# Kernel optimization log

Measured on AMD Instinct MI355X. Metric: run time of the kernel, lower is better.

Reference implementation:

```python
import jax, jax.numpy as jnp
import numpy as np

B, T, C = 2, 2048, 2048
H, HKV = 32, 8
D = C // H            # head_dim = 64
G = H // HKV          # groups = 4
ROPE_BASE = 10000.0


def _rotate_half(x):
    x1, x2 = jnp.split(x, 2, axis=-1)
    return jnp.concatenate((-x2, x1), axis=-1)


def _rope_tables(seq_len, dim):
    inv_freq = 1.0 / (ROPE_BASE ** (jnp.arange(0, dim, 2, dtype=jnp.float32) / dim))
    t = jnp.arange(seq_len, dtype=jnp.float32)
    freqs = jnp.outer(t, inv_freq)          # [T, D/2]
    emb = jnp.concatenate((freqs, freqs), axis=-1)  # [T, D]
    return jnp.cos(emb), jnp.sin(emb)


def setup_inputs() -> dict:
    key = jax.random.key(0)
    ks = jax.random.split(key, 5)
    s = 0.02
    return {
        "x": jax.random.normal(ks[0], (B, T, C), jnp.float32),
        "Wq": jax.random.normal(ks[1], (C, C), jnp.float32) * s,
        "Wk": jax.random.normal(ks[2], (HKV * D, C), jnp.float32) * s,
        "Wv": jax.random.normal(ks[3], (HKV * D, C), jnp.float32) * s,
        "Wo": jax.random.normal(ks[4], (C, C), jnp.float32) * s,
    }


def reference(x, Wq, Wk, Wv, Wo):
    b, t, c = x.shape
    # fused QKV projections (nn.Linear: y = x @ W.T)
    q = (x @ Wq.T).reshape(b, t, H, D).transpose(0, 2, 1, 3)      # [B,H,T,D]
    k = (x @ Wk.T).reshape(b, t, HKV, D).transpose(0, 2, 1, 3)    # [B,HKV,T,D]
    v = (x @ Wv.T).reshape(b, t, HKV, D).transpose(0, 2, 1, 3)

    # RoPE (start_pos = 0)
    cos, sin = _rope_tables(t, D)           # [T, D] each
    cos = cos[None, None]                   # [1,1,T,D]
    sin = sin[None, None]
    q = q * cos + _rotate_half(q) * sin
    k = k * cos + _rotate_half(k) * sin

    # GQA head expansion (repeat_interleave on head dim)
    k = jnp.repeat(k, G, axis=1)            # [B,H,T,D]
    v = jnp.repeat(v, G, axis=1)

    # causal attention
    scale = 1.0 / jnp.sqrt(jnp.asarray(D, jnp.float32))
    scores = jnp.einsum('bhqd,bhkd->bhqk', q, k) * scale          # [B,H,T,T]
    causal = jnp.tril(jnp.ones((t, t), dtype=bool))
    scores = jnp.where(causal[None, None], scores, -jnp.inf)
    attn = jax.nn.softmax(scores.astype(jnp.float32), axis=-1).astype(q.dtype)
    out = jnp.einsum('bhqk,bhkd->bhqd', attn, v)                  # [B,H,T,D]
    out = out.transpose(0, 2, 1, 3).reshape(b, t, c)
    return out @ Wo.T
```

## Files before the change

kernel.cpp:

```cpp
#include <hip/hip_runtime.h>
#include <hip/hip_bf16.h>
#include <math.h>

typedef short short8 __attribute__((ext_vector_type(8)));
typedef float floatx4 __attribute__((ext_vector_type(4)));

typedef __attribute__((address_space(1))) unsigned int as1_u32;
typedef __attribute__((address_space(3))) unsigned int as3_u32;

__device__ __forceinline__ void load_lds16(const void* g, void* l) {
  __builtin_amdgcn_global_load_lds((const as1_u32*)g, (as3_u32*)l, 16, 0, 0);
}

__device__ __forceinline__ unsigned short f2bf(float f) {
  __bf16 h = (__bf16)f;
  return __builtin_bit_cast(unsigned short, h);
}

#define TB 2
#define TT 2048
#define TC 2048
#define QKN 2560
#define KOFF 2048
#define SCALE_Q 0.18033688f

__global__ __launch_bounds__(256) void cast_all(
    const float* __restrict__ x, const float* __restrict__ wq,
    const float* __restrict__ wk, const float* __restrict__ wv,
    const float* __restrict__ wo,
    unsigned short* __restrict__ xb, unsigned short* __restrict__ wqkv,
    unsigned short* __restrict__ wob) {
  long i4 = (long)blockIdx.x * 256 + threadIdx.x;
  const float* src;
  unsigned short* dst;
  if (i4 < 2097152)      { src = x;  dst = xb; }
  else if (i4 < 3145728) { src = wq; dst = wqkv;           i4 -= 2097152; }
  else if (i4 < 3407872) { src = wk; dst = wqkv + 4194304; i4 -= 3145728; }
  else if (i4 < 3670016) { src = wv; dst = wqkv + 5242880; i4 -= 3407872; }
  else                   { src = wo; dst = wob;            i4 -= 3670016; }
  float4 v = ((const float4*)src)[i4];
  ushort4 o;
  o.x = f2bf(v.x); o.y = f2bf(v.y); o.z = f2bf(v.z); o.w = f2bf(v.w);
  ((ushort4*)dst)[i4] = o;
}

__global__ __launch_bounds__(256) void gemm_qkv(const unsigned short* __restrict__ A,
                                                const unsigned short* __restrict__ Bw,
                                                unsigned short* __restrict__ qk,
                                                unsigned short* __restrict__ vT) {
  __shared__ unsigned short As[128 * 64];
  __shared__ unsigned short Bs[128 * 64];
  const int K = 2048;
  const int tid = threadIdx.x;
  const int lane = tid & 63, w = tid >> 6;
  const int quad = lane >> 4, l15 = lane & 15;
  const int wm = w >> 1, wn = w & 1;
  const int m0 = blockIdx.y * 128, n0 = blockIdx.x * 128;

  floatx4 acc[4][4];
#pragma unroll
  for (int i = 0; i < 4; ++i)
#pragma unroll
    for (int j = 0; j < 4; ++j) acc[i][j] = (floatx4){0.f, 0.f, 0.f, 0.f};

  const int ar = tid >> 3;
  const int ac = (((tid & 7) ^ (ar & 7)) * 8);
  const unsigned short* Abase = A + (size_t)(m0 + ar) * K + ac;
  const unsigned short* Bbase = Bw + (size_t)(n0 + ar) * K + ac;

  for (int k0 = 0; k0 < K; k0 += 64) {
    __syncthreads();
#pragma unroll
    for (int p = 0; p < 4; ++p) {
      load_lds16(Abase + (size_t)(p * 32) * K + k0, (char*)As + p * 4096 + tid * 16);
      load_lds16(Bbase + (size_t)(p * 32) * K + k0, (char*)Bs + p * 4096 + tid * 16);
    }
    __syncthreads();
#pragma unroll
    for (int ks = 0; ks < 2; ++ks) {
      short8 af[4], bfr[4];
      const int key = (((ks << 2) + quad) ^ (l15 & 7)) << 4;
#pragma unroll
      for (int i = 0; i < 4; ++i)
        af[i] = *(const short8*)((const char*)As + (wm * 64 + i * 16 + l15) * 128 + key);
#pragma unroll
      for (int j = 0; j < 4; ++j)
        bfr[j] = *(const short8*)((const char*)Bs + (wn * 64 + j * 16 + l15) * 128 + key);
#pragma unroll
      for (int i = 0; i < 4; ++i)
#pragma unroll
        for (int j = 0; j < 4; ++j)
          acc[i][j] = __builtin_amdgcn_mfma_f32_16x16x32_bf16(af[i], bfr[j], acc[i][j], 0, 0, 0);
    }
  }

  const int colb = n0 + wn * 64;
  if (colb < QKN) {
    const float qscale = (colb < KOFF) ? SCALE_Q : 1.0f;
#pragma unroll
    for (int i = 0; i < 4; ++i) {
      const int rowb = m0 + wm * 64 + i * 16 + quad * 4;
      const int tb = rowb & (TT - 1);
#pragma unroll
      for (int j = 0; j < 2; ++j) {
        const int col = colb + j * 16 + l15;
        const int d = j * 16 + l15;
        const float inv = exp2f((float)d * -0.4152410119f);
#pragma unroll
        for (int r = 0; r < 4; ++r) {
          float sn, cs;
          sincosf((float)(tb + r) * inv, &sn, &cs);
          const float a = acc[i][j][r], b2 = acc[i][j + 2][r];
          const float qa = (a * cs - b2 * sn) * qscale;
          const float qb = (b2 * cs + a * sn) * qscale;
          unsigned short* p = qk + (size_t)(rowb + r) * QKN + col;
          p[0] = f2bf(qa);
          p[32] = f2bf(qb);
        }
      }
    }
  } else {
#pragma unroll
    for (int i = 0; i < 4; ++i) {
      const int rowb = m0 + wm * 64 + i * 16 + quad * 4;
#pragma unroll
      for (int j = 0; j < 4; ++j) {
        const int col = colb + j * 16 + l15;
        ushort4 pk;
        pk.x = f2bf(acc[i][j][0]); pk.y = f2bf(acc[i][j][1]);
        pk.z = f2bf(acc[i][j][2]); pk.w = f2bf(acc[i][j][3]);
        *(ushort4*)(vT + (size_t)(col - 2560) * 4096 + rowb) = pk;
      }
    }
  }
}

__global__ __launch_bounds__(256) void gemm_nt_f32(const unsigned short* __restrict__ A,
                                                   const unsigned short* __restrict__ Bw,
                                                   float* __restrict__ C,
                                                   int M, int N, int K) {
  __shared__ unsigned short As[128 * 64];
  __shared__ unsigned short Bs[128 * 64];
  const int tid = threadIdx.x;
  const int lane = tid & 63, w = tid >> 6;
  const int quad = lane >> 4, l15 = lane & 15;
  const int wm = w >> 1, wn = w & 1;
  const int m0 = blockIdx.y * 128, n0 = blockIdx.x * 128;

  floatx4 acc[4][4];
#pragma unroll
  for (int i = 0; i < 4; ++i)
#pragma unroll
    for (int j = 0; j < 4; ++j) acc[i][j] = (floatx4){0.f, 0.f, 0.f, 0.f};

  const int ar = tid >> 3;
  const int ac = (((tid & 7) ^ (ar & 7)) * 8);
  const unsigned short* Abase = A + (size_t)(m0 + ar) * K + ac;
  const unsigned short* Bbase = Bw + (size_t)(n0 + ar) * K + ac;

  for (int k0 = 0; k0 < K; k0 += 64) {
    __syncthreads();
#pragma unroll
    for (int p = 0; p < 4; ++p) {
      load_lds16(Abase + (size_t)(p * 32) * K + k0, (char*)As + p * 4096 + tid * 16);
      load_lds16(Bbase + (size_t)(p * 32) * K + k0, (char*)Bs + p * 4096 + tid * 16);
    }
    __syncthreads();
#pragma unroll
    for (int ks = 0; ks < 2; ++ks) {
      short8 af[4], bfr[4];
      const int key = (((ks << 2) + quad) ^ (l15 & 7)) << 4;
#pragma unroll
      for (int i = 0; i < 4; ++i)
        af[i] = *(const short8*)((const char*)As + (wm * 64 + i * 16 + l15) * 128 + key);
#pragma unroll
      for (int j = 0; j < 4; ++j)
        bfr[j] = *(const short8*)((const char*)Bs + (wn * 64 + j * 16 + l15) * 128 + key);
#pragma unroll
      for (int i = 0; i < 4; ++i)
#pragma unroll
        for (int j = 0; j < 4; ++j)
          acc[i][j] = __builtin_amdgcn_mfma_f32_16x16x32_bf16(af[i], bfr[j], acc[i][j], 0, 0, 0);
    }
  }
#pragma unroll
  for (int i = 0; i < 4; ++i) {
    const int row = m0 + wm * 64 + i * 16 + quad * 4;
#pragma unroll
    for (int j = 0; j < 4; ++j) {
      const int col = n0 + wn * 64 + j * 16 + l15;
#pragma unroll
      for (int r = 0; r < 4; ++r)
        C[(size_t)(row + r) * N + col] = acc[i][j][r];
    }
  }
}

#define LDSA_K(buf) (lds + (buf) * 8192)
#define LDSA_V(buf) (lds + 16384 + (buf) * 8192)
#define LDSA_P      (lds + 32768)

__global__ __launch_bounds__(256) void attn_kernel(const unsigned short* __restrict__ qk,
                                                   const unsigned short* __restrict__ vT,
                                                   unsigned short* __restrict__ attn) {
  const int bx = blockIdx.x;
  const int h = blockIdx.y, b = blockIdx.z;
  const int hk = h >> 2;
  const int tid = threadIdx.x;
  const int w = tid >> 6, lane = tid & 63, quad = lane >> 4, l15 = lane & 15;

  __shared__ char lds[51200];
  unsigned short* Pq = (unsigned short*)(LDSA_P + w * 4608);

  const int srow = tid >> 3;
  const int sgrp = ((tid & 7) ^ (srow & 7));

  const short8 ones = {16256, 16256, 16256, 16256, 16256, 16256, 16256, 16256};

  for (int pass = 0; pass < 2; ++pass) {
    const int qt = pass ? (15 - bx) : bx;
    const size_t rowQ = (size_t)(b * TT + qt * 128);

    {
      const unsigned short* qsrc = qk + (rowQ + srow) * QKN + h * 64 + sgrp * 8;
#pragma unroll
      for (int p = 0; p < 4; ++p)
        load_lds16(qsrc + (size_t)p * 32 * QKN, lds + p * 4096 + tid * 16);
    }
    __syncthreads();
    short8 qf[2][2];
#pragma unroll
    for (int i = 0; i < 2; ++i)
#pragma unroll
      for (int ks = 0; ks < 2; ++ks)
        qf[i][ks] = *(const short8*)(lds + (w * 32 + i * 16 + l15) * 128 +
                                     ((((ks << 2) + quad) ^ (l15 & 7)) << 4));
    __syncthreads();

    floatx4 accO[2][4], accL[2];
#pragma unroll
    for (int i = 0; i < 2; ++i) {
      accL[i] = (floatx4){0.f, 0.f, 0.f, 0.f};
#pragma unroll
      for (int j = 0; j < 4; ++j) accO[i][j] = (floatx4){0.f, 0.f, 0.f, 0.f};
    }

    {
      const unsigned short* ksrc =
          qk + (size_t)(b * TT + srow) * QKN + KOFF + hk * 64 + sgrp * 8;
      load_lds16(ksrc, LDSA_K(0) + tid * 16);
      load_lds16(ksrc + (size_t)32 * QKN, LDSA_K(0) + 4096 + tid * 16);
      const unsigned short* vsrc =
          vT + (size_t)(hk * 64 + srow) * 4096 + b * TT + sgrp * 8;
      load_lds16(vsrc, LDSA_V(0) + tid * 16);
      load_lds16(vsrc + (size_t)32 * 4096, LDSA_V(0) + 4096 + tid * 16);
    }
    __syncthreads();

    const int ktmax = 2 * qt + 1;
    for (int kt = 0; kt <= ktmax; ++kt) {
      const int cur = kt & 1, nxt = cur ^ 1;
      if (kt < ktmax) {
        const unsigned short* ksrc =
            qk + (size_t)(b * TT + (kt + 1) * 64 + srow) * QKN + KOFF + hk * 64 + sgrp * 8;
        load_lds16(ksrc, LDSA_K(nxt) + tid * 16);
        load_lds16(ksrc + (size_t)32 * QKN, LDSA_K(nxt) + 4096 + tid * 16);
        const unsigned short* vsrc =
            vT + (size_t)(hk * 64 + srow) * 4096 + b * TT + (kt + 1) * 64 + sgrp * 8;
        load_lds16(vsrc, LDSA_V(nxt) + tid * 16);
        load_lds16(vsrc + (size_t)32 * 4096, LDSA_V(nxt) + 4096 + tid * 16);
      }

      const char* Ks = LDSA_K(cur);
      floatx4 st[2][4];
#pragma unroll
      for (int jm = 0; jm < 4; ++jm) {
        const int krow = jm * 16 + l15;
        const short8 kf0 = *(const short8*)(Ks + krow * 128 + ((quad ^ (l15 & 7)) << 4));
        const short8 kf1 = *(const short8*)(Ks + krow * 128 + (((4 + quad) ^ (l15 & 7)) << 4));
#pragma unroll
        for (int i = 0; i < 2; ++i) {
          floatx4 z = (floatx4){0.f, 0.f, 0.f, 0.f};
          z = __builtin_amdgcn_mfma_f32_16x16x32_bf16(kf0, qf[i][0], z, 0, 0, 0);
          st[i][jm] = __builtin_amdgcn_mfma_f32_16x16x32_bf16(kf1, qf[i][1], z, 0, 0, 0);
        }
      }

      const bool domask = (kt >= 2 * qt);
#pragma unroll
      for (int i = 0; i < 2; ++i) {
        const int qg = qt * 128 + w * 32 + i * 16 + l15;
#pragma unroll
        for (int jm = 0; jm < 4; ++jm) {
          float e0 = exp2f(st[i][jm][0]);
          float e1 = exp2f(st[i][jm][1]);
          float e2 = exp2f(st[i][jm][2]);
          float e3 = exp2f(st[i][jm][3]);
          if (domask) {
            const int kg = kt * 64 + jm * 16 + quad * 4;
            if (kg > qg) e0 = 0.f;
            if (kg + 1 > qg) e1 = 0.f;
            if (kg + 2 > qg) e2 = 0.f;
            if (kg + 3 > qg) e3 = 0.f;
          }
          ushort4 pk;
          pk.x = f2bf(e0); pk.y = f2bf(e1); pk.z = f2bf(e2); pk.w = f2bf(e3);
          *(ushort4*)(Pq + (i * 16 + l15) * 72 + jm * 16 + quad * 4) = pk;
        }
      }
      asm volatile("s_waitcnt lgkmcnt(0)" ::: "memory");

      const char* Vt = LDSA_V(cur);
#pragma unroll
      for (int ks = 0; ks < 2; ++ks) {
        short8 pf[2];
#pragma unroll
        for (int i2 = 0; i2 < 2; ++i2)
          pf[i2] = *(const short8*)(Pq + (i2 * 16 + l15) * 72 + ks * 32 + quad * 8);
        accL[0] = __builtin_amdgcn_mfma_f32_16x16x32_bf16(pf[0], ones, accL[0], 0, 0, 0);
        accL[1] = __builtin_amdgcn_mfma_f32_16x16x32_bf16(pf[1], ones, accL[1], 0, 0, 0);
#pragma unroll
        for (int jd = 0; jd < 4; ++jd) {
          const int d = jd * 16 + l15;
          const short8 vf = *(const short8*)(Vt + d * 128 +
                                             ((((ks << 2) + quad) ^ (l15 & 7)) << 4));
          accO[0][jd] = __builtin_amdgcn_mfma_f32_16x16x32_bf16(pf[0], vf, accO[0][jd], 0, 0, 0);
          accO[1][jd] = __builtin_amdgcn_mfma_f32_16x16x32_bf16(pf[1], vf, accO[1][jd], 0, 0, 0);
        }
      }
      __syncthreads();
    }

#pragma unroll
    for (int i2 = 0; i2 < 2; ++i2) {
#pragma unroll
      for (int jd = 0; jd < 4; ++jd) {
        const int col = h * 64 + jd * 16 + l15;
#pragma unroll
        for (int r = 0; r < 4; ++r) {
          const size_t row = rowQ + w * 32 + i2 * 16 + quad * 4 + r;
          attn[row * TC + col] = f2bf(accO[i2][jd][r] / accL[i2][r]);
        }
      }
    }
  }
}

extern "C" void kernel_launch(void* const* d_in, const int* in_sizes, int n_in,
                              void* d_out, int out_size, void* d_ws, size_t ws_size,
                              hipStream_t stream) {
  const float* x = (const float*)d_in[0];
  const float* Wq = (const float*)d_in[1];
  const float* Wk = (const float*)d_in[2];
  const float* Wv = (const float*)d_in[3];
  const float* Wo = (const float*)d_in[4];
  float* out = (float*)d_out;

  char* ws = (char*)d_ws;
  unsigned short* xb   = (unsigned short*)(ws);
  unsigned short* wqkv = (unsigned short*)(ws + 16777216);
  unsigned short* wob  = (unsigned short*)(ws + 29360128);
  unsigned short* qk   = (unsigned short*)(ws + 37748736);
  unsigned short* vT   = (unsigned short*)(ws + 58720256);
  unsigned short* attn = (unsigned short*)(ws + 62914560);

  cast_all<<<18432, 256, 0, stream>>>(x, Wq, Wk, Wv, Wo, xb, wqkv, wob);
  gemm_qkv<<<dim3(24, 32), 256, 0, stream>>>(xb, wqkv, qk, vT);
  attn_kernel<<<dim3(8, 32, 2), 256, 0, stream>>>(qk, vT, attn);
  gemm_nt_f32<<<dim3(16, 32), 256, 0, stream>>>(attn, wob, out, 4096, TC, 2048);
}
```

Before: 300.8 us.

## Precompute RoPE table and remap block indices for cache-friendly XCD scheduling

Computes a cos/sin RoPE table once inside the cast kernel and has the QKV GEMM epilogue read it instead of calling sincosf per element. It also remaps the linear block IDs in both GEMMs and the attention kernel. Blocks that share the same A rows or the same KV head then land on the same XCD (assuming round-robin dispatch across 8 XCDs), which improves L2 reuse. The table reuses the attention-output workspace region, which is safe only because attention writes there after the GEMM has consumed the table.

Result: no change. 297.9 us (-1.0%).

```diff
diff --git a/kernel.cpp b/kernel.cpp
--- a/kernel.cpp
+++ b/kernel.cpp
@@ -29,7 +29,15 @@
     const float* __restrict__ wk, const float* __restrict__ wv,
     const float* __restrict__ wo,
     unsigned short* __restrict__ xb, unsigned short* __restrict__ wqkv,
-    unsigned short* __restrict__ wob) {
+    unsigned short* __restrict__ wob, float2* __restrict__ ropeTab) {
+  if (blockIdx.x < 256) {
+    const int idx = blockIdx.x * 256 + threadIdx.x;
+    const int t = idx >> 5, d = idx & 31;
+    const float inv = exp2f((float)d * -0.4152410119f);
+    float sn, cs;
+    sincosf((float)t * inv, &sn, &cs);
+    ropeTab[idx] = make_float2(cs, sn);
+  }
   long i4 = (long)blockIdx.x * 256 + threadIdx.x;
   const float* src;
   unsigned short* dst;
@@ -47,7 +55,8 @@
 __global__ __launch_bounds__(256) void gemm_qkv(const unsigned short* __restrict__ A,
                                                 const unsigned short* __restrict__ Bw,
                                                 unsigned short* __restrict__ qk,
-                                                unsigned short* __restrict__ vT) {
+                                                unsigned short* __restrict__ vT,
+                                                const float2* __restrict__ ropeTab) {
   __shared__ unsigned short As[128 * 64];
   __shared__ unsigned short Bs[128 * 64];
   const int K = 2048;
@@ -55,7 +64,10 @@
   const int lane = tid & 63, w = tid >> 6;
   const int quad = lane >> 4, l15 = lane & 15;
   const int wm = w >> 1, wn = w & 1;
-  const int m0 = blockIdx.y * 128, n0 = blockIdx.x * 128;
+  const int lin = blockIdx.y * 24 + blockIdx.x;
+  const int sub = lin >> 3;
+  const int m0 = (sub / 3) * 128;
+  const int n0 = ((lin & 7) * 3 + sub % 3) * 128;
 
   floatx4 acc[4][4];
 #pragma unroll
@@ -105,14 +117,12 @@
       for (int j = 0; j < 2; ++j) {
         const int col = colb + j * 16 + l15;
         const int d = j * 16 + l15;
-        const float inv = exp2f((float)d * -0.4152410119f);
 #pragma unroll
         for (int r = 0; r < 4; ++r) {
-          float sn, cs;
-          sincosf((float)(tb + r) * inv, &sn, &cs);
+          const float2 cssn = ropeTab[(tb + r) * 32 + d];
           const float a = acc[i][j][r], b2 = acc[i][j + 2][r];
-          const float qa = (a * cs - b2 * sn) * qscale;
-          const float qb = (b2 * cs + a * sn) * qscale;
+          const float qa = (a * cssn.x - b2 * cssn.y) * qscale;
+          const float qb = (b2 * cssn.x + a * cssn.y) * qscale;
           unsigned short* p = qk + (size_t)(rowb + r) * QKN + col;
           p[0] = f2bf(qa);
           p[32] = f2bf(qb);
@@ -145,7 +155,10 @@
   const int lane = tid & 63, w = tid >> 6;
   const int quad = lane >> 4, l15 = lane & 15;
   const int wm = w >> 1, wn = w & 1;
-  const int m0 = blockIdx.y * 128, n0 = blockIdx.x * 128;
+  const int lin = blockIdx.y * 16 + blockIdx.x;
+  const int sub = lin >> 3;
+  const int m0 = (sub >> 1) * 128;
+  const int n0 = ((lin & 7) * 2 + (sub & 1)) * 128;
 
   floatx4 acc[4][4];
 #pragma unroll
@@ -203,8 +216,10 @@
 __global__ __launch_bounds__(256) void attn_kernel(const unsigned short* __restrict__ qk,
                                                    const unsigned short* __restrict__ vT,
                                                    unsigned short* __restrict__ attn) {
-  const int bx = blockIdx.x;
-  const int h = blockIdx.y, b = blockIdx.z;
+  const int hcode = blockIdx.x;
+  const int h = (hcode & 7) * 4 + (hcode >> 3);
+  const int bx = blockIdx.y;
+  const int b = blockIdx.z;
   const int hk = h >> 2;
   const int tid = threadIdx.x;
   const int w = tid >> 6, lane = tid & 63, quad = lane >> 4, l15 = lane & 15;
@@ -363,9 +378,10 @@
   unsigned short* qk   = (unsigned short*)(ws + 37748736);
   unsigned short* vT   = (unsigned short*)(ws + 58720256);
   unsigned short* attn = (unsigned short*)(ws + 62914560);
-
-  cast_all<<<18432, 256, 0, stream>>>(x, Wq, Wk, Wv, Wo, xb, wqkv, wob);
-  gemm_qkv<<<dim3(24, 32), 256, 0, stream>>>(xb, wqkv, qk, vT);
-  attn_kernel<<<dim3(8, 32, 2), 256, 0, stream>>>(qk, vT, attn);
+  float2* ropeTab = (float2*)(ws + 62914560);
+
+  cast_all<<<18432, 256, 0, stream>>>(x, Wq, Wk, Wv, Wo, xb, wqkv, wob, ropeTab);
+  gemm_qkv<<<dim3(24, 32), 256, 0, stream>>>(xb, wqkv, qk, vT, ropeTab);
+  attn_kernel<<<dim3(32, 8, 2), 256, 0, stream>>>(qk, vT, attn);
   gemm_nt_f32<<<dim3(16, 32), 256, 0, stream>>>(attn, wob, out, 4096, TC, 2048);
 }
```
